# Performance work log

Hardware: AMD Instinct MI355X
Metric: run time of the kernel (lower is better)

The kernel has to match this reference:

```python
import jax, jax.numpy as jnp
import numpy as np
from jax import lax

EPS = 1e-5  # GroupNorm eps (torch default)

def _silu(x):
    return x * jax.nn.sigmoid(x)

def _conv1x1(x, w, b):
    # x: (N, Ci, H, W), w: (Co, Ci), b: (Co,)
    return jnp.einsum('oi,nihw->nohw', w, x) + b[None, :, None, None]

def _conv3x3(x, w, b):
    # x: (N, Ci, H, W), w: (Co, Ci, 3, 3)
    y = lax.conv_general_dilated(x, w, window_strides=(1, 1), padding='SAME',
                                 dimension_numbers=('NCHW', 'OIHW', 'NCHW'))
    return y + b[None, :, None, None]

def setup_inputs() -> dict:
    key = jax.random.key(0)
    ks = jax.random.split(key, 6)
    B, C, H, W = 32, 512, 64, 64
    cg = 16
    return {
        'x': jax.random.normal(ks[0], (B, C, H, W), dtype=jnp.float32),
        'w1': jax.random.normal(ks[1], (cg, cg), dtype=jnp.float32) * 0.1,
        'b1': jnp.zeros((cg,), jnp.float32),
        'wh': jax.random.normal(ks[2], (cg, cg), dtype=jnp.float32) * 0.1,
        'bh': jnp.zeros((cg,), jnp.float32),
        'ww': jax.random.normal(ks[3], (cg, cg), dtype=jnp.float32) * 0.1,
        'bw': jnp.zeros((cg,), jnp.float32),
        'w3': jax.random.normal(ks[4], (cg, cg, 3, 3), dtype=jnp.float32) * 0.1,
        'b3': jnp.zeros((cg,), jnp.float32),
        'gamma': jnp.ones((cg,), jnp.float32),
        'beta': jnp.zeros((cg,), jnp.float32),
    }

def reference(x, w1, b1, wh, bh, ww, bw, w3, b3, gamma, beta):
    b, c, h, w = x.shape
    cg = w1.shape[0]
    g = c // cg
    n = b * g
    hw = h * w
    xg = x.reshape(n, cg, h, w)
    # directional pooling: (N, cg, H, 1) and (N, cg, W, 1)
    x_h = jnp.mean(xg, axis=3, keepdims=True)
    x_w = jnp.transpose(jnp.mean(xg, axis=2, keepdims=True), (0, 1, 3, 2))
    y = jnp.concatenate([x_h, x_w], axis=2)            # (N, cg, H+W, 1)
    y = _silu(_conv1x1(y, w1, b1))
    y_h, y_w = y[:, :, :h, :], y[:, :, h:, :]
    y_w = jnp.transpose(y_w, (0, 1, 3, 2))             # (N, cg, 1, W)
    a_h = jax.nn.sigmoid(_conv1x1(y_h, wh, bh))        # (N, cg, H, 1)
    a_w = jax.nn.sigmoid(_conv1x1(y_w, ww, bw))        # (N, cg, 1, W)
    x1 = xg * a_h * a_w
    # GroupNorm(num_groups=1): normalize over (cg, H, W) per sample
    mu = jnp.mean(x1, axis=(1, 2, 3), keepdims=True)
    var = jnp.var(x1, axis=(1, 2, 3), keepdims=True)
    x1 = (x1 - mu) * lax.rsqrt(var + EPS)
    x1 = x1 * gamma[None, :, None, None] + beta[None, :, None, None]
    x3 = _silu(_conv3x3(xg, w3, b3))
    A1 = jax.nn.softmax(x1.reshape(n, cg, hw), axis=-1)
    A3 = jax.nn.softmax(x3.reshape(n, cg, hw), axis=-1)
    v1 = jnp.mean(x1, axis=(2, 3))                     # (N, cg)
    v3 = jnp.mean(x3, axis=(2, 3))                     # (N, cg)
    s1 = jnp.einsum('nc,ncp->np', v1, A3)              # (N, HW)
    s2 = jnp.einsum('nc,ncp->np', v3, A1)
    s = jax.nn.sigmoid(s1 + s2).reshape(n, 1, h, w)
    out = (xg * s).reshape(b, c, h, w)
    return out
```

## Files before the change

### kernel.cpp

```cpp
#include <hip/hip_runtime.h>


typedef short bf16x8 __attribute__((ext_vector_type(8)));
typedef float f32x4 __attribute__((ext_vector_type(4)));

__device__ __forceinline__ unsigned short f2bf(float f) {
    union { float f; unsigned int u; } v; v.f = f;
    unsigned int u = v.u;
    u += 0x7fffu + ((u >> 16) & 1u);
    return (unsigned short)(u >> 16);
}
__device__ __forceinline__ float bf2f(unsigned short h) {
    union { unsigned int u; float f; } v; v.u = ((unsigned int)h) << 16;
    return v.f;
}
__device__ __forceinline__ float sigm(float v) { return 1.0f / (1.0f + __expf(-v)); }

#define XIDX(h1,w1,c) ((((h1)*2 + ((c)>>3))*66 + (w1))*8 + ((c)&7))

__global__ __launch_bounds__(512) void ema_fused(
    const float* __restrict__ x,
    const float* __restrict__ w1, const float* __restrict__ b1,
    const float* __restrict__ wh, const float* __restrict__ bh,
    const float* __restrict__ ww, const float* __restrict__ bw,
    const float* __restrict__ w3, const float* __restrict__ b3,
    const float* __restrict__ gamma, const float* __restrict__ beta,
    float* __restrict__ out)
{
    const int n   = blockIdx.x;
    const int tid = threadIdx.x;
    const int lane = tid & 63;
    const int wv   = tid >> 6;
    const int qd   = lane >> 4;
    const int col  = lane & 15;

    const float* xg = x + (size_t)n * 65536;
    unsigned int* ob = (unsigned int*)out + (size_t)n * 65536;

    __shared__ unsigned short sX[69696];
    __shared__ float sG[2048];
    __shared__ float sRedA[128], sRedB[128], sRedC[128], sRedD[128];
    __shared__ float sS1[16], sSQ[16], sMn[16], sMx[16], sM3[16], sS3[16];
    __shared__ float sA[16], sB1[16], sQ1[16], sQ3[16];
    __shared__ float sScal[2];

    for (int i = tid; i < 34848; i += 512) ((unsigned int*)sX)[i] = 0u;
    __syncthreads();
    for (int e = tid; e < 32768; e += 512) {
        int c2 = e & 7, w = (e >> 3) & 63, r = e >> 9;
        float v0 = xg[(2*c2)*4096 + r*64 + w];
        float v1 = xg[(2*c2+1)*4096 + r*64 + w];
        unsigned int pk = (unsigned int)f2bf(v0) | ((unsigned int)f2bf(v1) << 16);
        ((unsigned int*)sX)[XIDX(r+1, w+1, 2*c2) >> 1] = pk;
    }
    __syncthreads();

    if (tid < 256) {
        int half = tid & 1;
        int idx  = tid >> 1;
        int isCol = idx >> 6;
        int rc = idx & 63;
        float acc[8] = {0,0,0,0,0,0,0,0};
        for (int t = 0; t < 64; ++t) {
            int hh = isCol ? (t + 1) : (rc + 1);
            int wwi = isCol ? (rc + 1) : (t + 1);
            const bf16x8 v = *(const bf16x8*)&sX[XIDX(hh, wwi, half*8)];
            #pragma unroll
            for (int j = 0; j < 8; ++j) acc[j] += bf2f((unsigned short)v[j]);
        }
        #pragma unroll
        for (int j = 0; j < 8; ++j)
            sG[isCol*1024 + (half*8+j)*64 + rc] = acc[j] * (1.0f/64.0f);
    }
    __syncthreads();

    {
        float yv[4];
        #pragma unroll
        for (int j = 0; j < 4; ++j) {
            int tsk = tid + j*512;
            int o = tsk & 15, q = tsk >> 4;
            float acc = b1[o];
            #pragma unroll
            for (int i = 0; i < 16; ++i)
                acc += w1[o*16 + i] * sG[((q>>6)<<10) + i*64 + (q & 63)];
            yv[j] = acc * sigm(acc);
        }
        __syncthreads();
        #pragma unroll
        for (int j = 0; j < 4; ++j) {
            int tsk = tid + j*512;
            int o = tsk & 15, q = tsk >> 4;
            sG[o*128 + q] = yv[j];
        }
    }
    __syncthreads();
    {
        float av[4];
        #pragma unroll
        for (int j = 0; j < 4; ++j) {
            int tsk = tid + j*512;
            int kind = tsk >> 10;
            int o = tsk & 15, pos = (tsk >> 4) & 63;
            const float* wm = kind ? ww : wh;
            float acc = kind ? bw[o] : bh[o];
            #pragma unroll
            for (int i = 0; i < 16; ++i)
                acc += wm[o*16 + i] * sG[i*128 + kind*64 + pos];
            av[j] = sigm(acc);
        }
        __syncthreads();
        #pragma unroll
        for (int j = 0; j < 4; ++j) {
            int tsk = tid + j*512;
            int kind = tsk >> 10, o = tsk & 15, pos = (tsk >> 4) & 63;
            sG[kind*1024 + o*64 + pos] = av[j];
        }
    }
    __syncthreads();

    {
        bf16x8 afr[5];
        int offs[5];
        #pragma unroll
        for (int mm = 0; mm < 5; ++mm) {
            int t = 2*mm + (qd >> 1);
            #pragma unroll
            for (int j = 0; j < 8; ++j) {
                int i = ((qd & 1) << 3) + j;
                float v = (t <= 8) ? w3[(col*16 + i)*9 + t] : 0.0f;
                afr[mm][j] = (short)f2bf(v);
            }
            int tb = (t > 8) ? 8 : t;
            int dy = tb/3 - 1, dx = tb - (tb/3)*3 - 1;
            offs[mm] = dy*1056 + dx*8;
        }
        float b3v[4];
        #pragma unroll
        for (int r = 0; r < 4; ++r) b3v[r] = b3[qd*4 + r];

        float tmax[4] = {-1e30f,-1e30f,-1e30f,-1e30f};
        float tsum[4] = {0.f,0.f,0.f,0.f};

        for (int k = 0; k < 32; ++k) {
            int tile = wv*32 + k;
            int h = tile >> 2, wq = tile & 3;
            int base = XIDX(h+1, wq*16 + col + 1, (qd & 1)*8);
            f32x4 acc = {0.f, 0.f, 0.f, 0.f};
            #pragma unroll
            for (int mm = 0; mm < 5; ++mm) {
                const bf16x8 bfr = *(const bf16x8*)&sX[base + offs[mm]];
                acc = __builtin_amdgcn_mfma_f32_16x16x32_bf16(afr[mm], bfr, acc, 0, 0, 0);
            }
            int p = h*64 + wq*16 + col;
            float xv[4];
            #pragma unroll
            for (int r = 0; r < 4; ++r) {
                float v = acc[r] + b3v[r];
                float sv = v * sigm(v);
                xv[r] = sv;
                tmax[r] = fmaxf(tmax[r], sv);
                tsum[r] += sv;
            }
            unsigned int u0 = (unsigned int)f2bf(xv[0]) | ((unsigned int)f2bf(xv[1]) << 16);
            unsigned int u1 = (unsigned int)f2bf(xv[2]) | ((unsigned int)f2bf(xv[3]) << 16);
            ob[(4*qd)*4096 + p]     = u0;
            ob[(4*qd + 2)*4096 + p] = u1;
        }
        #pragma unroll
        for (int m = 1; m < 16; m <<= 1) {
            #pragma unroll
            for (int r = 0; r < 4; ++r) {
                tmax[r] = fmaxf(tmax[r], __shfl_xor(tmax[r], m, 64));
                tsum[r] += __shfl_xor(tsum[r], m, 64);
            }
        }
        if (col == 0) {
            #pragma unroll
            for (int r = 0; r < 4; ++r) {
                sRedA[wv*16 + qd*4 + r] = tmax[r];
                sRedB[wv*16 + qd*4 + r] = tsum[r];
            }
        }
    }
    __syncthreads();
    if (tid < 16) {
        float mx = -1e30f, sm = 0.f;
        for (int v2 = 0; v2 < 8; ++v2) { mx = fmaxf(mx, sRedA[v2*16 + tid]); sm += sRedB[v2*16 + tid]; }
        sM3[tid] = mx; sS3[tid] = sm;
    }
    __syncthreads();

    {
        int half = tid & 1;
        int wq4  = (tid >> 1) & 3;
        int r    = tid >> 3;
        float ah8[8];
        #pragma unroll
        for (int j = 0; j < 8; ++j) ah8[j] = sG[(half*8+j)*64 + r];
        float s1[8], q1[8], mn[8], mx[8];
        #pragma unroll
        for (int j = 0; j < 8; ++j) { s1[j]=0.f; q1[j]=0.f; mn[j]=1e30f; mx[j]=-1e30f; }
        for (int wi = 0; wi < 16; ++wi) {
            int w = wq4*16 + wi;
            const bf16x8 v = *(const bf16x8*)&sX[XIDX(r+1, w+1, half*8)];
            #pragma unroll
            for (int j = 0; j < 8; ++j) {
                float aw = sG[1024 + (half*8+j)*64 + w];
                float x1 = bf2f((unsigned short)v[j]) * ah8[j] * aw;
                s1[j] += x1; q1[j] += x1*x1;
                mn[j] = fminf(mn[j], x1); mx[j] = fmaxf(mx[j], x1);
            }
        }
        #pragma unroll
        for (int m = 2; m < 64; m <<= 1) {
            #pragma unroll
            for (int j = 0; j < 8; ++j) {
                s1[j] += __shfl_xor(s1[j], m, 64);
                q1[j] += __shfl_xor(q1[j], m, 64);
                mn[j] = fminf(mn[j], __shfl_xor(mn[j], m, 64));
                mx[j] = fmaxf(mx[j], __shfl_xor(mx[j], m, 64));
            }
        }
        if ((lane >> 1) == 0) {
            #pragma unroll
            for (int j = 0; j < 8; ++j) {
                int c = half*8 + j;
                sRedA[wv*16 + c] = s1[j];
                sRedB[wv*16 + c] = q1[j];
                sRedC[wv*16 + c] = mn[j];
                sRedD[wv*16 + c] = mx[j];
            }
        }
    }
    __syncthreads();
    if (tid < 16) {
        float s=0.f, q=0.f, mn=1e30f, mx=-1e30f;
        for (int v2 = 0; v2 < 8; ++v2) {
            s += sRedA[v2*16+tid]; q += sRedB[v2*16+tid];
            mn = fminf(mn, sRedC[v2*16+tid]); mx = fmaxf(mx, sRedD[v2*16+tid]);
        }
        sS1[tid]=s; sSQ[tid]=q; sMn[tid]=mn; sMx[tid]=mx;
    }
    __syncthreads();
    if (tid == 0) {
        float S=0.f, Q=0.f;
        for (int c = 0; c < 16; ++c) { S += sS1[c]; Q += sSQ[c]; }
        float mu = S * (1.0f/65536.0f);
        float var = Q * (1.0f/65536.0f) - mu*mu;
        sScal[0] = mu; sScal[1] = rsqrtf(var + 1e-5f);
    }
    __syncthreads();
    if (tid < 16) {
        float mu = sScal[0], rstd = sScal[1];
        float a  = gamma[tid] * rstd;
        float bb = beta[tid] - mu * a;
        float m1 = (a >= 0.f) ? (a*sMx[tid] + bb) : (a*sMn[tid] + bb);
        sA[tid]  = a;
        sB1[tid] = bb - m1;
        sMn[tid] = a * (sS1[tid] * (1.0f/4096.0f)) + bb;
        sMx[tid] = sS3[tid] * (1.0f/4096.0f);
    }
    __syncthreads();

    {
        float z1[16], z3[16];
        #pragma unroll
        for (int c = 0; c < 16; ++c) { z1[c]=0.f; z3[c]=0.f; }
        for (int pp = 0; pp < 8; ++pp) {
            int p = pp*512 + tid;
            int h = p >> 6, w = p & 63;
            const bf16x8 v0 = *(const bf16x8*)&sX[XIDX(h+1, w+1, 0)];
            const bf16x8 v1 = *(const bf16x8*)&sX[XIDX(h+1, w+1, 8)];
            unsigned int xq[8];
            #pragma unroll
            for (int c2 = 0; c2 < 8; ++c2) xq[c2] = ob[(2*c2)*4096 + p];
            #pragma unroll
            for (int c = 0; c < 16; ++c) {
                float xv = bf2f((unsigned short)((c < 8) ? v0[c] : v1[c-8]));
                float g = sG[c*64 + h] * sG[1024 + c*64 + w];
                z1[c] += __expf(xv*g*sA[c] + sB1[c]);
                unsigned short ub = (unsigned short)((c & 1) ? (xq[c>>1] >> 16) : (xq[c>>1] & 0xffffu));
                z3[c] += __expf(bf2f(ub) - sM3[c]);
            }
        }
        #pragma unroll
        for (int m = 1; m < 64; m <<= 1) {
            #pragma unroll
            for (int c = 0; c < 16; ++c) {
                z1[c] += __shfl_xor(z1[c], m, 64);
                z3[c] += __shfl_xor(z3[c], m, 64);
            }
        }
        if (lane == 0) {
            #pragma unroll
            for (int c = 0; c < 16; ++c) { sRedA[wv*16 + c] = z1[c]; sRedB[wv*16 + c] = z3[c]; }
        }
    }
    __syncthreads();
    if (tid < 16) {
        float a1=0.f, a3=0.f;
        for (int v2 = 0; v2 < 8; ++v2) { a1 += sRedA[v2*16+tid]; a3 += sRedB[v2*16+tid]; }
        sQ1[tid] = sMx[tid] / a1;
        sQ3[tid] = sMn[tid] / a3;
    }
    __syncthreads();

    for (int pp = 0; pp < 8; ++pp) {
        int p = pp*512 + tid;
        int h = p >> 6, w = p & 63;
        const bf16x8 v0 = *(const bf16x8*)&sX[XIDX(h+1, w+1, 0)];
        const bf16x8 v1 = *(const bf16x8*)&sX[XIDX(h+1, w+1, 8)];
        unsigned int xq[8];
        #pragma unroll
        for (int c2 = 0; c2 < 8; ++c2) xq[c2] = ob[(2*c2)*4096 + p];
        float xf[16];
        #pragma unroll
        for (int c = 0; c < 16; ++c) xf[c] = xg[c*4096 + p];
        float z = 0.f;
        #pragma unroll
        for (int c = 0; c < 16; ++c) {
            float xv = bf2f((unsigned short)((c < 8) ? v0[c] : v1[c-8]));
            float g = sG[c*64 + h] * sG[1024 + c*64 + w];
            float e1 = __expf(xv*g*sA[c] + sB1[c]);
            unsigned short ub = (unsigned short)((c & 1) ? (xq[c>>1] >> 16) : (xq[c>>1] & 0xffffu));
            float e3 = __expf(bf2f(ub) - sM3[c]);
            z += sQ3[c]*e3 + sQ1[c]*e1;
        }
        float s = 1.0f / (1.0f + __expf(-z));
        #pragma unroll
        for (int c = 0; c < 16; ++c)
            ob[c*4096 + p] = __float_as_uint(xf[c] * s);
    }
}

extern "C" void kernel_launch(void* const* d_in, const int* in_sizes, int n_in,
                              void* d_out, int out_size, void* d_ws, size_t ws_size,
                              hipStream_t stream) {
    const float* x     = (const float*)d_in[0];
    const float* w1    = (const float*)d_in[1];
    const float* b1    = (const float*)d_in[2];
    const float* wh    = (const float*)d_in[3];
    const float* bh    = (const float*)d_in[4];
    const float* ww    = (const float*)d_in[5];
    const float* bw    = (const float*)d_in[6];
    const float* w3    = (const float*)d_in[7];
    const float* b3    = (const float*)d_in[8];
    const float* gamma = (const float*)d_in[9];
    const float* beta  = (const float*)d_in[10];
    hipLaunchKernelGGL(ema_fused, dim3(1024), dim3(512), 0, stream,
                       x, w1, b1, wh, bh, ww, bw, w3, b3, gamma, beta, (float*)d_out);
}
```

Measured before the change: 726.8 us.

## Stream input through small row-chunk LDS tile instead of caching whole slab

Replaces the ~139KB bf16 LDS copy of the full 16x64x64 group with a 18-row sliding tile, processing the image in four 16-row chunks. Row and column pooling are computed on the fly, and the conv3x3 MFMA runs per chunk. Later passes read x from global memory in fp32 with vectorized float4 loads instead of reading the bf16 LDS copy. The much smaller LDS footprint and launch_bounds(512,4) are meant to allow several blocks per CU, at the cost of re-reading x from global/L2 in the later passes and extra barriers per chunk.

```diff
diff --git a/kernel.cpp b/kernel.cpp
--- a/kernel.cpp
+++ b/kernel.cpp
@@ -3,6 +3,7 @@
 
 typedef short bf16x8 __attribute__((ext_vector_type(8)));
 typedef float f32x4 __attribute__((ext_vector_type(4)));
+typedef unsigned int u32x4 __attribute__((ext_vector_type(4)));
 
 __device__ __forceinline__ unsigned short f2bf(float f) {
     union { float f; unsigned int u; } v; v.f = f;
@@ -16,9 +17,9 @@
 }
 __device__ __forceinline__ float sigm(float v) { return 1.0f / (1.0f + __expf(-v)); }
 
-#define XIDX(h1,w1,c) ((((h1)*2 + ((c)>>3))*66 + (w1))*8 + ((c)&7))
-
-__global__ __launch_bounds__(512) void ema_fused(
+#define CIDX(lr, w1, c) ((((lr)*2 + ((c)>>3))*66 + (w1))*8 + ((c)&7))
+
+__global__ __launch_bounds__(512, 4) void ema_fused(
     const float* __restrict__ x,
     const float* __restrict__ w1, const float* __restrict__ b1,
     const float* __restrict__ wh, const float* __restrict__ bh,
@@ -27,8 +28,8 @@
     const float* __restrict__ gamma, const float* __restrict__ beta,
     float* __restrict__ out)
 {
-    const int n   = blockIdx.x;
-    const int tid = threadIdx.x;
+    const int n    = blockIdx.x;
+    const int tid  = threadIdx.x;
     const int lane = tid & 63;
     const int wv   = tid >> 6;
     const int qd   = lane >> 4;
@@ -37,40 +38,166 @@
     const float* xg = x + (size_t)n * 65536;
     unsigned int* ob = (unsigned int*)out + (size_t)n * 65536;
 
-    __shared__ unsigned short sX[69696];
-    __shared__ float sG[2048];
-    __shared__ float sRedA[128], sRedB[128], sRedC[128], sRedD[128];
+    __shared__ __align__(16) unsigned short sT[19008];
+    __shared__ __align__(16) float sG[2048];
+    __shared__ float sRowP[1024];
+    __shared__ float sRedA[128], sRedB[128];
     __shared__ float sS1[16], sSQ[16], sMn[16], sMx[16], sM3[16], sS3[16];
     __shared__ float sA[16], sB1[16], sQ1[16], sQ3[16];
     __shared__ float sScal[2];
 
-    for (int i = tid; i < 34848; i += 512) ((unsigned int*)sX)[i] = 0u;
-    __syncthreads();
-    for (int e = tid; e < 32768; e += 512) {
-        int c2 = e & 7, w = (e >> 3) & 63, r = e >> 9;
-        float v0 = xg[(2*c2)*4096 + r*64 + w];
-        float v1 = xg[(2*c2+1)*4096 + r*64 + w];
-        unsigned int pk = (unsigned int)f2bf(v0) | ((unsigned int)f2bf(v1) << 16);
-        ((unsigned int*)sX)[XIDX(r+1, w+1, 2*c2) >> 1] = pk;
-    }
-    __syncthreads();
-
-    if (tid < 256) {
-        int half = tid & 1;
-        int idx  = tid >> 1;
-        int isCol = idx >> 6;
-        int rc = idx & 63;
-        float acc[8] = {0,0,0,0,0,0,0,0};
-        for (int t = 0; t < 64; ++t) {
-            int hh = isCol ? (t + 1) : (rc + 1);
-            int wwi = isCol ? (rc + 1) : (t + 1);
-            const bf16x8 v = *(const bf16x8*)&sX[XIDX(hh, wwi, half*8)];
-            #pragma unroll
-            for (int j = 0; j < 8; ++j) acc[j] += bf2f((unsigned short)v[j]);
-        }
-        #pragma unroll
-        for (int j = 0; j < 8; ++j)
-            sG[isCol*1024 + (half*8+j)*64 + rc] = acc[j] * (1.0f/64.0f);
+    sG[tid] = 0.f; sG[tid + 512] = 0.f;
+    if (tid < 72) {
+        int lr = tid >> 2, blk = (tid >> 1) & 1, w1 = (tid & 1) * 65;
+        f32x4 zz = {0.f, 0.f, 0.f, 0.f};
+        *(f32x4*)&sT[((lr*2 + blk)*66 + w1)*8] = zz;
+    }
+
+    bf16x8 afr[5];
+    int offs[5];
+    #pragma unroll
+    for (int mm = 0; mm < 5; ++mm) {
+        int t = 2*mm + (qd >> 1);
+        #pragma unroll
+        for (int j = 0; j < 8; ++j) {
+            int i = ((qd & 1) << 3) + j;
+            float v = (t <= 8) ? w3[(col*16 + i)*9 + t] : 0.0f;
+            afr[mm][j] = (short)f2bf(v);
+        }
+        int tb = (t > 8) ? 8 : t;
+        int dy = tb/3 - 1, dx = tb - (tb/3)*3 - 1;
+        offs[mm] = dy*1056 + dx*8;
+    }
+    float b3v[4];
+    #pragma unroll
+    for (int r = 0; r < 4; ++r) b3v[r] = b3[qd*4 + r];
+
+    float tmax[4] = {-1e30f,-1e30f,-1e30f,-1e30f};
+    float tsum[4] = {0.f,0.f,0.f,0.f};
+    float colacc[8] = {0.f,0.f,0.f,0.f,0.f,0.f,0.f,0.f};
+    const int sblk = (tid >> 6) & 1;
+    const int sw   = tid & 63;
+
+    __syncthreads();
+
+    for (int c0 = 0; c0 < 4; ++c0) {
+        #pragma unroll
+        for (int k = 0; k < 5; ++k) {
+            int t = k*512 + tid;
+            if (t < 2304) {
+                int lr = t >> 7;
+                int gr = (c0 << 4) + lr - 1;
+                float v[8];
+                if ((unsigned)gr < 64u) {
+                    #pragma unroll
+                    for (int j = 0; j < 8; ++j)
+                        v[j] = xg[(sblk*8 + j)*4096 + gr*64 + sw];
+                } else {
+                    #pragma unroll
+                    for (int j = 0; j < 8; ++j) v[j] = 0.f;
+                }
+                if ((unsigned)(lr - 1) < 16u) {
+                    #pragma unroll
+                    for (int j = 0; j < 8; ++j) colacc[j] += v[j];
+                }
+                u32x4 pk;
+                #pragma unroll
+                for (int m = 0; m < 4; ++m)
+                    pk[m] = (unsigned int)f2bf(v[2*m]) | ((unsigned int)f2bf(v[2*m+1]) << 16);
+                *(u32x4*)&sT[((lr*2 + sblk)*66 + (sw + 1))*8] = pk;
+            }
+        }
+        __syncthreads();
+
+        if (tid < 128) {
+            int rr = tid >> 3, chalf = (tid >> 2) & 1, wq = tid & 3;
+            float racc[8] = {0.f,0.f,0.f,0.f,0.f,0.f,0.f,0.f};
+            #pragma unroll 4
+            for (int wi = 0; wi < 16; ++wi) {
+                const bf16x8 vv = *(const bf16x8*)&sT[CIDX(rr + 1, wq*16 + wi + 1, chalf*8)];
+                #pragma unroll
+                for (int j = 0; j < 8; ++j) racc[j] += bf2f((unsigned short)vv[j]);
+            }
+            #pragma unroll
+            for (int j = 0; j < 8; ++j)
+                sRowP[((rr*2 + chalf)*4 + wq)*8 + j] = racc[j];
+        }
+        #pragma unroll
+        for (int k = 0; k < 8; ++k) {
+            int tile = wv*8 + k;
+            int hl = tile >> 2, wq = tile & 3;
+            int base = CIDX(hl + 1, wq*16 + col + 1, (qd & 1)*8);
+            f32x4 acc = {0.f, 0.f, 0.f, 0.f};
+            #pragma unroll
+            for (int mm = 0; mm < 5; ++mm) {
+                const bf16x8 bfr = *(const bf16x8*)&sT[base + offs[mm]];
+                acc = __builtin_amdgcn_mfma_f32_16x16x32_bf16(afr[mm], bfr, acc, 0, 0, 0);
+            }
+            int p = ((c0 << 4) + hl)*64 + wq*16 + col;
+            float xv4[4];
+            #pragma unroll
+            for (int r = 0; r < 4; ++r) {
+                float v = acc[r] + b3v[r];
+                float sv = v * sigm(v);
+                xv4[r] = sv;
+                tmax[r] = fmaxf(tmax[r], sv);
+                tsum[r] += sv;
+            }
+            ob[(4*qd)*4096 + p]     = (unsigned int)f2bf(xv4[0]) | ((unsigned int)f2bf(xv4[1]) << 16);
+            ob[(4*qd + 2)*4096 + p] = (unsigned int)f2bf(xv4[2]) | ((unsigned int)f2bf(xv4[3]) << 16);
+        }
+        __syncthreads();
+
+        if (tid < 256) {
+            int c = tid & 15, rr = tid >> 4;
+            int bse = (rr*2 + (c >> 3))*4;
+            float s = sRowP[(bse + 0)*8 + (c & 7)] + sRowP[(bse + 1)*8 + (c & 7)]
+                    + sRowP[(bse + 2)*8 + (c & 7)] + sRowP[(bse + 3)*8 + (c & 7)];
+            sG[c*64 + (c0 << 4) + rr] += s;
+        }
+    }
+
+    #pragma unroll
+    for (int m = 1; m < 16; m <<= 1) {
+        #pragma unroll
+        for (int r = 0; r < 4; ++r) {
+            tmax[r] = fmaxf(tmax[r], __shfl_xor(tmax[r], m, 64));
+            tsum[r] += __shfl_xor(tsum[r], m, 64);
+        }
+    }
+    if (col == 0) {
+        #pragma unroll
+        for (int r = 0; r < 4; ++r) {
+            sRedA[wv*16 + qd*4 + r] = tmax[r];
+            sRedB[wv*16 + qd*4 + r] = tsum[r];
+        }
+    }
+    {
+        float* colScr = (float*)sT;
+        f32x4 d0 = {colacc[0], colacc[1], colacc[2], colacc[3]};
+        f32x4 d1 = {colacc[4], colacc[5], colacc[6], colacc[7]};
+        *(f32x4*)&colScr[tid*8]     = d0;
+        *(f32x4*)&colScr[tid*8 + 4] = d1;
+    }
+    __syncthreads();
+
+    {
+        const float* colScr = (const float*)sT;
+        #pragma unroll
+        for (int s0 = 0; s0 < 2; ++s0) {
+            int s = s0*512 + tid;
+            int c = s >> 6, w = s & 63;
+            int off = (c >> 3)*64 + w;
+            float cs = colScr[(off      )*8 + (c & 7)] + colScr[(off + 128)*8 + (c & 7)]
+                     + colScr[(off + 256)*8 + (c & 7)] + colScr[(off + 384)*8 + (c & 7)];
+            sG[1024 + s] = cs * (1.0f/64.0f);
+            sG[s] *= (1.0f/64.0f);
+        }
+    }
+    if (tid < 16) {
+        float mx = -1e30f, sm = 0.f;
+        for (int v2 = 0; v2 < 8; ++v2) { mx = fmaxf(mx, sRedA[v2*16 + tid]); sm += sRedB[v2*16 + tid]; }
+        sM3[tid] = mx; sS3[tid] = sm;
     }
     __syncthreads();
 
@@ -120,131 +247,37 @@
     __syncthreads();
 
     {
-        bf16x8 afr[5];
-        int offs[5];
-        #pragma unroll
-        for (int mm = 0; mm < 5; ++mm) {
-            int t = 2*mm + (qd >> 1);
-            #pragma unroll
-            for (int j = 0; j < 8; ++j) {
-                int i = ((qd & 1) << 3) + j;
-                float v = (t <= 8) ? w3[(col*16 + i)*9 + t] : 0.0f;
-                afr[mm][j] = (short)f2bf(v);
-            }
-            int tb = (t > 8) ? 8 : t;
-            int dy = tb/3 - 1, dx = tb - (tb/3)*3 - 1;
-            offs[mm] = dy*1056 + dx*8;
-        }
-        float b3v[4];
-        #pragma unroll
-        for (int r = 0; r < 4; ++r) b3v[r] = b3[qd*4 + r];
-
-        float tmax[4] = {-1e30f,-1e30f,-1e30f,-1e30f};
-        float tsum[4] = {0.f,0.f,0.f,0.f};
-
-        for (int k = 0; k < 32; ++k) {
-            int tile = wv*32 + k;
-            int h = tile >> 2, wq = tile & 3;
-            int base = XIDX(h+1, wq*16 + col + 1, (qd & 1)*8);
-            f32x4 acc = {0.f, 0.f, 0.f, 0.f};
-            #pragma unroll
-            for (int mm = 0; mm < 5; ++mm) {
-                const bf16x8 bfr = *(const bf16x8*)&sX[base + offs[mm]];
-                acc = __builtin_amdgcn_mfma_f32_16x16x32_bf16(afr[mm], bfr, acc, 0, 0, 0);
-            }
-            int p = h*64 + wq*16 + col;
-            float xv[4];
-            #pragma unroll
-            for (int r = 0; r < 4; ++r) {
-                float v = acc[r] + b3v[r];
-                float sv = v * sigm(v);
-                xv[r] = sv;
-                tmax[r] = fmaxf(tmax[r], sv);
-                tsum[r] += sv;
-            }
-            unsigned int u0 = (unsigned int)f2bf(xv[0]) | ((unsigned int)f2bf(xv[1]) << 16);
-            unsigned int u1 = (unsigned int)f2bf(xv[2]) | ((unsigned int)f2bf(xv[3]) << 16);
-            ob[(4*qd)*4096 + p]     = u0;
-            ob[(4*qd + 2)*4096 + p] = u1;
-        }
-        #pragma unroll
-        for (int m = 1; m < 16; m <<= 1) {
-            #pragma unroll
-            for (int r = 0; r < 4; ++r) {
-                tmax[r] = fmaxf(tmax[r], __shfl_xor(tmax[r], m, 64));
-                tsum[r] += __shfl_xor(tsum[r], m, 64);
-            }
-        }
-        if (col == 0) {
-            #pragma unroll
-            for (int r = 0; r < 4; ++r) {
-                sRedA[wv*16 + qd*4 + r] = tmax[r];
-                sRedB[wv*16 + qd*4 + r] = tsum[r];
-            }
-        }
-    }
-    __syncthreads();
-    if (tid < 16) {
-        float mx = -1e30f, sm = 0.f;
-        for (int v2 = 0; v2 < 8; ++v2) { mx = fmaxf(mx, sRedA[v2*16 + tid]); sm += sRedB[v2*16 + tid]; }
-        sM3[tid] = mx; sS3[tid] = sm;
-    }
-    __syncthreads();
-
-    {
-        int half = tid & 1;
-        int wq4  = (tid >> 1) & 3;
-        int r    = tid >> 3;
-        float ah8[8];
-        #pragma unroll
-        for (int j = 0; j < 8; ++j) ah8[j] = sG[(half*8+j)*64 + r];
-        float s1[8], q1[8], mn[8], mx[8];
-        #pragma unroll
-        for (int j = 0; j < 8; ++j) { s1[j]=0.f; q1[j]=0.f; mn[j]=1e30f; mx[j]=-1e30f; }
-        for (int wi = 0; wi < 16; ++wi) {
-            int w = wq4*16 + wi;
-            const bf16x8 v = *(const bf16x8*)&sX[XIDX(r+1, w+1, half*8)];
-            #pragma unroll
-            for (int j = 0; j < 8; ++j) {
-                float aw = sG[1024 + (half*8+j)*64 + w];
-                float x1 = bf2f((unsigned short)v[j]) * ah8[j] * aw;
-                s1[j] += x1; q1[j] += x1*x1;
-                mn[j] = fminf(mn[j], x1); mx[j] = fmaxf(mx[j], x1);
-            }
-        }
-        #pragma unroll
-        for (int m = 2; m < 64; m <<= 1) {
-            #pragma unroll
-            for (int j = 0; j < 8; ++j) {
-                s1[j] += __shfl_xor(s1[j], m, 64);
-                q1[j] += __shfl_xor(q1[j], m, 64);
-                mn[j] = fminf(mn[j], __shfl_xor(mn[j], m, 64));
-                mx[j] = fmaxf(mx[j], __shfl_xor(mx[j], m, 64));
-            }
-        }
-        if ((lane >> 1) == 0) {
-            #pragma unroll
-            for (int j = 0; j < 8; ++j) {
-                int c = half*8 + j;
-                sRedA[wv*16 + c] = s1[j];
-                sRedB[wv*16 + c] = q1[j];
-                sRedC[wv*16 + c] = mn[j];
-                sRedD[wv*16 + c] = mx[j];
-            }
-        }
-    }
-    __syncthreads();
-    if (tid < 16) {
-        float s=0.f, q=0.f, mn=1e30f, mx=-1e30f;
-        for (int v2 = 0; v2 < 8; ++v2) {
-            s += sRedA[v2*16+tid]; q += sRedB[v2*16+tid];
-            mn = fminf(mn, sRedC[v2*16+tid]); mx = fmaxf(mx, sRedD[v2*16+tid]);
-        }
-        sS1[tid]=s; sSQ[tid]=q; sMn[tid]=mn; sMx[tid]=mx;
+        #pragma unroll
+        for (int cc = 0; cc < 2; ++cc) {
+            const int c = wv*2 + cc;
+            const int w0 = (lane & 15) * 4;
+            const f32x4 aw4 = *(const f32x4*)&sG[1024 + c*64 + w0];
+            float ps = 0.f, pq = 0.f, mn = 1e30f, mx = -1e30f;
+            #pragma unroll 4
+            for (int i = 0; i < 16; ++i) {
+                const int p = i*256 + lane*4;
+                const float ah = sG[c*64 + i*4 + (lane >> 4)];
+                const f32x4 xv = *(const f32x4*)&xg[c*4096 + p];
+                #pragma unroll
+                for (int j = 0; j < 4; ++j) {
+                    float x1 = xv[j] * ah * aw4[j];
+                    ps += x1; pq = fmaf(x1, x1, pq);
+                    mn = fminf(mn, x1); mx = fmaxf(mx, x1);
+                }
+            }
+            #pragma unroll
+            for (int m = 1; m < 64; m <<= 1) {
+                ps += __shfl_xor(ps, m, 64);
+                pq += __shfl_xor(pq, m, 64);
+                mn = fminf(mn, __shfl_xor(mn, m, 64));
+                mx = fmaxf(mx, __shfl_xor(mx, m, 64));
+            }
+            if (lane == 0) { sS1[c] = ps; sSQ[c] = pq; sMn[c] = mn; sMx[c] = mx; }
+        }
     }
     __syncthreads();
     if (tid == 0) {
-        float S=0.f, Q=0.f;
+        float S = 0.f, Q = 0.f;
         for (int c = 0; c < 16; ++c) { S += sS1[c]; Q += sSQ[c]; }
         float mu = S * (1.0f/65536.0f);
         float var = Q * (1.0f/65536.0f) - mu*mu;
@@ -266,22 +299,30 @@
     {
         float z1[16], z3[16];
         #pragma unroll
-        for (int c = 0; c < 16; ++c) { z1[c]=0.f; z3[c]=0.f; }
-        for (int pp = 0; pp < 8; ++pp) {
-            int p = pp*512 + tid;
-            int h = p >> 6, w = p & 63;
-            const bf16x8 v0 = *(const bf16x8*)&sX[XIDX(h+1, w+1, 0)];
-            const bf16x8 v1 = *(const bf16x8*)&sX[XIDX(h+1, w+1, 8)];
-            unsigned int xq[8];
-            #pragma unroll
-            for (int c2 = 0; c2 < 8; ++c2) xq[c2] = ob[(2*c2)*4096 + p];
-            #pragma unroll
-            for (int c = 0; c < 16; ++c) {
-                float xv = bf2f((unsigned short)((c < 8) ? v0[c] : v1[c-8]));
-                float g = sG[c*64 + h] * sG[1024 + c*64 + w];
-                z1[c] += __expf(xv*g*sA[c] + sB1[c]);
-                unsigned short ub = (unsigned short)((c & 1) ? (xq[c>>1] >> 16) : (xq[c>>1] & 0xffffu));
-                z3[c] += __expf(bf2f(ub) - sM3[c]);
+        for (int c = 0; c < 16; ++c) { z1[c] = 0.f; z3[c] = 0.f; }
+        #pragma unroll
+        for (int it = 0; it < 2; ++it) {
+            const int p0 = it*2048 + tid*4;
+            const int h  = p0 >> 6;
+            const int w0 = (tid & 15)*4;
+            #pragma unroll
+            for (int c2 = 0; c2 < 8; ++c2) {
+                const u32x4 xq = *(const u32x4*)&ob[(2*c2)*4096 + p0];
+                #pragma unroll
+                for (int hf = 0; hf < 2; ++hf) {
+                    const int c = 2*c2 + hf;
+                    const f32x4 xf  = *(const f32x4*)&xg[c*4096 + p0];
+                    const f32x4 aw4 = *(const f32x4*)&sG[1024 + c*64 + w0];
+                    const float tt = sG[c*64 + h] * sA[c];
+                    const float bb = sB1[c];
+                    const float m3 = sM3[c];
+                    #pragma unroll
+                    for (int j = 0; j < 4; ++j) {
+                        z1[c] += __expf(fmaf(xf[j], tt * aw4[j], bb));
+                        unsigned int uu = hf ? (xq[j] & 0xffff0000u) : (xq[j] << 16);
+                        z3[c] += __expf(__uint_as_float(uu) - m3);
+                    }
+                }
             }
         }
         #pragma unroll
@@ -299,38 +340,51 @@
     }
     __syncthreads();
     if (tid < 16) {
-        float a1=0.f, a3=0.f;
-        for (int v2 = 0; v2 < 8; ++v2) { a1 += sRedA[v2*16+tid]; a3 += sRedB[v2*16+tid]; }
+        float a1 = 0.f, a3 = 0.f;
+        for (int v2 = 0; v2 < 8; ++v2) { a1 += sRedA[v2*16 + tid]; a3 += sRedB[v2*16 + tid]; }
         sQ1[tid] = sMx[tid] / a1;
         sQ3[tid] = sMn[tid] / a3;
     }
     __syncthreads();
 
-    for (int pp = 0; pp < 8; ++pp) {
-        int p = pp*512 + tid;
-        int h = p >> 6, w = p & 63;
-        const bf16x8 v0 = *(const bf16x8*)&sX[XIDX(h+1, w+1, 0)];
-        const bf16x8 v1 = *(const bf16x8*)&sX[XIDX(h+1, w+1, 8)];
-        unsigned int xq[8];
-        #pragma unroll
-        for (int c2 = 0; c2 < 8; ++c2) xq[c2] = ob[(2*c2)*4096 + p];
-        float xf[16];
-        #pragma unroll
-        for (int c = 0; c < 16; ++c) xf[c] = xg[c*4096 + p];
-        float z = 0.f;
+    #pragma unroll
+    for (int it = 0; it < 2; ++it) {
+        const int p0 = it*2048 + tid*4;
+        const int h  = p0 >> 6;
+        const int w0 = (tid & 15)*4;
+        f32x4 z = {0.f, 0.f, 0.f, 0.f};
+        #pragma unroll
+        for (int c2 = 0; c2 < 8; ++c2) {
+            const u32x4 xq = *(const u32x4*)&ob[(2*c2)*4096 + p0];
+            #pragma unroll
+            for (int hf = 0; hf < 2; ++hf) {
+                const int c = 2*c2 + hf;
+                const f32x4 xf  = *(const f32x4*)&xg[c*4096 + p0];
+                const f32x4 aw4 = *(const f32x4*)&sG[1024 + c*64 + w0];
+                const float tt = sG[c*64 + h] * sA[c];
+                const float bb = sB1[c];
+                const float m3 = sM3[c];
+                const float q1c = sQ1[c], q3c = sQ3[c];
+                #pragma unroll
+                for (int j = 0; j < 4; ++j) {
+                    float e1 = __expf(fmaf(xf[j], tt * aw4[j], bb));
+                    unsigned int uu = hf ? (xq[j] & 0xffff0000u) : (xq[j] << 16);
+                    float e3 = __expf(__uint_as_float(uu) - m3);
+                    z[j] = fmaf(q1c, e1, fmaf(q3c, e3, z[j]));
+                }
+            }
+        }
+        f32x4 s4;
+        #pragma unroll
+        for (int j = 0; j < 4; ++j) s4[j] = 1.0f / (1.0f + __expf(-z[j]));
         #pragma unroll
         for (int c = 0; c < 16; ++c) {
-            float xv = bf2f((unsigned short)((c < 8) ? v0[c] : v1[c-8]));
-            float g = sG[c*64 + h] * sG[1024 + c*64 + w];
-            float e1 = __expf(xv*g*sA[c] + sB1[c]);
-            unsigned short ub = (unsigned short)((c & 1) ? (xq[c>>1] >> 16) : (xq[c>>1] & 0xffffu));
-            float e3 = __expf(bf2f(ub) - sM3[c]);
-            z += sQ3[c]*e3 + sQ1[c]*e1;
-        }
-        float s = 1.0f / (1.0f + __expf(-z));
-        #pragma unroll
-        for (int c = 0; c < 16; ++c)
-            ob[c*4096 + p] = __float_as_uint(xf[c] * s);
+            const f32x4 xf = *(const f32x4*)&xg[c*4096 + p0];
+            u32x4 o4;
+            #pragma unroll
+            for (int j = 0; j < 4; ++j) o4[j] = __float_as_uint(xf[j] * s4[j]);
+            *(u32x4*)&ob[c*4096 + p0] = o4;
+        }
     }
 }
 
```

New measurement: 1.355 ms. +86.4%, slower.

## Recompute 3x3 conv via MFMA per pass instead of spilling bf16 to output

Applied to the files above, without the earlier changes.

Doubles the block to 1024 threads and stops staging the conv3x3+SiLU result as bf16 in the global output buffer. The MFMA convolution is instead recomputed in each of the three passes (stats, softmax denominators, final write). The GroupNorm statistics are folded into the first conv pass, and the row/column pooling is split across more threads. This removes global scratch writes and reads, at the cost of three times the MFMA work and higher register pressure at 1024 threads per block.

```diff
diff --git a/kernel.cpp b/kernel.cpp
--- a/kernel.cpp
+++ b/kernel.cpp
@@ -2,6 +2,7 @@
 
 
 typedef short bf16x8 __attribute__((ext_vector_type(8)));
+typedef short bf16x4 __attribute__((ext_vector_type(4)));
 typedef float f32x4 __attribute__((ext_vector_type(4)));
 
 __device__ __forceinline__ unsigned short f2bf(float f) {
@@ -18,7 +19,7 @@
 
 #define XIDX(h1,w1,c) ((((h1)*2 + ((c)>>3))*66 + (w1))*8 + ((c)&7))
 
-__global__ __launch_bounds__(512) void ema_fused(
+__global__ __launch_bounds__(1024) void ema_fused(
     const float* __restrict__ x,
     const float* __restrict__ w1, const float* __restrict__ b1,
     const float* __restrict__ wh, const float* __restrict__ bh,
@@ -27,41 +28,61 @@
     const float* __restrict__ gamma, const float* __restrict__ beta,
     float* __restrict__ out)
 {
-    const int n   = blockIdx.x;
-    const int tid = threadIdx.x;
+    const int n    = blockIdx.x;
+    const int tid  = threadIdx.x;
     const int lane = tid & 63;
     const int wv   = tid >> 6;
     const int qd   = lane >> 4;
     const int col  = lane & 15;
 
     const float* xg = x + (size_t)n * 65536;
-    unsigned int* ob = (unsigned int*)out + (size_t)n * 65536;
-
-    __shared__ unsigned short sX[69696];
-    __shared__ float sG[2048];
-    __shared__ float sRedA[128], sRedB[128], sRedC[128], sRedD[128];
+    float* ob = out + (size_t)n * 65536;
+
+    __shared__ __align__(16) unsigned short sX[69696];
+    __shared__ __align__(16) float sG[2048];
+    __shared__ float sRedA[256], sRedB[256], sRedC[256], sRedD[256], sRedE[256], sRedF[256];
     __shared__ float sS1[16], sSQ[16], sMn[16], sMx[16], sM3[16], sS3[16];
     __shared__ float sA[16], sB1[16], sQ1[16], sQ3[16];
     __shared__ float sScal[2];
 
-    for (int i = tid; i < 34848; i += 512) ((unsigned int*)sX)[i] = 0u;
-    __syncthreads();
-    for (int e = tid; e < 32768; e += 512) {
+    for (int i = tid; i < 34848; i += 1024) ((unsigned int*)sX)[i] = 0u;
+    __syncthreads();
+    for (int e = tid; e < 32768; e += 1024) {
         int c2 = e & 7, w = (e >> 3) & 63, r = e >> 9;
         float v0 = xg[(2*c2)*4096 + r*64 + w];
         float v1 = xg[(2*c2+1)*4096 + r*64 + w];
         unsigned int pk = (unsigned int)f2bf(v0) | ((unsigned int)f2bf(v1) << 16);
         ((unsigned int*)sX)[XIDX(r+1, w+1, 2*c2) >> 1] = pk;
     }
-    __syncthreads();
-
-    if (tid < 256) {
+
+    bf16x8 afr[5];
+    int offs[5];
+    #pragma unroll
+    for (int mm = 0; mm < 5; ++mm) {
+        int t = 2*mm + (qd >> 1);
+        #pragma unroll
+        for (int j = 0; j < 8; ++j) {
+            int i = ((qd & 1) << 3) + j;
+            float v = (t <= 8) ? w3[(col*16 + i)*9 + t] : 0.0f;
+            afr[mm][j] = (short)f2bf(v);
+        }
+        int tb = (t > 8) ? 8 : t;
+        int dy = tb/3 - 1, dx = tb - (tb/3)*3 - 1;
+        offs[mm] = dy*1056 + dx*8;
+    }
+    float b3v[4];
+    #pragma unroll
+    for (int r = 0; r < 4; ++r) b3v[r] = b3[qd*4 + r];
+    __syncthreads();
+
+    if (tid < 512) {
         int half = tid & 1;
-        int idx  = tid >> 1;
+        int part = (tid >> 1) & 1;
+        int idx  = tid >> 2;
         int isCol = idx >> 6;
         int rc = idx & 63;
         float acc[8] = {0,0,0,0,0,0,0,0};
-        for (int t = 0; t < 64; ++t) {
+        for (int t = part*32; t < part*32 + 32; ++t) {
             int hh = isCol ? (t + 1) : (rc + 1);
             int wwi = isCol ? (rc + 1) : (t + 1);
             const bf16x8 v = *(const bf16x8*)&sX[XIDX(hh, wwi, half*8)];
@@ -69,16 +90,20 @@
             for (int j = 0; j < 8; ++j) acc[j] += bf2f((unsigned short)v[j]);
         }
         #pragma unroll
-        for (int j = 0; j < 8; ++j)
-            sG[isCol*1024 + (half*8+j)*64 + rc] = acc[j] * (1.0f/64.0f);
-    }
-    __syncthreads();
-
-    {
-        float yv[4];
-        #pragma unroll
-        for (int j = 0; j < 4; ++j) {
-            int tsk = tid + j*512;
+        for (int j = 0; j < 8; ++j) acc[j] += __shfl_xor(acc[j], 2, 64);
+        if (part == 0) {
+            #pragma unroll
+            for (int j = 0; j < 8; ++j)
+                sG[isCol*1024 + (half*8+j)*64 + rc] = acc[j] * (1.0f/64.0f);
+        }
+    }
+    __syncthreads();
+
+    {
+        float yv[2];
+        #pragma unroll
+        for (int j = 0; j < 2; ++j) {
+            int tsk = tid + j*1024;
             int o = tsk & 15, q = tsk >> 4;
             float acc = b1[o];
             #pragma unroll
@@ -88,18 +113,18 @@
         }
         __syncthreads();
         #pragma unroll
-        for (int j = 0; j < 4; ++j) {
-            int tsk = tid + j*512;
+        for (int j = 0; j < 2; ++j) {
+            int tsk = tid + j*1024;
             int o = tsk & 15, q = tsk >> 4;
             sG[o*128 + q] = yv[j];
         }
     }
     __syncthreads();
     {
-        float av[4];
-        #pragma unroll
-        for (int j = 0; j < 4; ++j) {
-            int tsk = tid + j*512;
+        float av[2];
+        #pragma unroll
+        for (int j = 0; j < 2; ++j) {
+            int tsk = tid + j*1024;
             int kind = tsk >> 10;
             int o = tsk & 15, pos = (tsk >> 4) & 63;
             const float* wm = kind ? ww : wh;
@@ -111,8 +136,8 @@
         }
         __syncthreads();
         #pragma unroll
-        for (int j = 0; j < 4; ++j) {
-            int tsk = tid + j*512;
+        for (int j = 0; j < 2; ++j) {
+            int tsk = tid + j*1024;
             int kind = tsk >> 10, o = tsk & 15, pos = (tsk >> 4) & 63;
             sG[kind*1024 + o*64 + pos] = av[j];
         }
@@ -120,52 +145,33 @@
     __syncthreads();
 
     {
-        bf16x8 afr[5];
-        int offs[5];
-        #pragma unroll
-        for (int mm = 0; mm < 5; ++mm) {
-            int t = 2*mm + (qd >> 1);
-            #pragma unroll
-            for (int j = 0; j < 8; ++j) {
-                int i = ((qd & 1) << 3) + j;
-                float v = (t <= 8) ? w3[(col*16 + i)*9 + t] : 0.0f;
-                afr[mm][j] = (short)f2bf(v);
-            }
-            int tb = (t > 8) ? 8 : t;
-            int dy = tb/3 - 1, dx = tb - (tb/3)*3 - 1;
-            offs[mm] = dy*1056 + dx*8;
-        }
-        float b3v[4];
-        #pragma unroll
-        for (int r = 0; r < 4; ++r) b3v[r] = b3[qd*4 + r];
-
         float tmax[4] = {-1e30f,-1e30f,-1e30f,-1e30f};
         float tsum[4] = {0.f,0.f,0.f,0.f};
-
-        for (int k = 0; k < 32; ++k) {
-            int tile = wv*32 + k;
-            int h = tile >> 2, wq = tile & 3;
-            int base = XIDX(h+1, wq*16 + col + 1, (qd & 1)*8);
+        float s1[4] = {0.f,0.f,0.f,0.f}, q1[4] = {0.f,0.f,0.f,0.f};
+        float mn[4] = {1e30f,1e30f,1e30f,1e30f}, mx[4] = {-1e30f,-1e30f,-1e30f,-1e30f};
+        for (int k = 0; k < 16; ++k) {
+            int tile = wv*16 + k;
+            int hl = tile >> 2, wq = tile & 3;
+            int w = wq*16 + col;
+            int base = XIDX(hl+1, w+1, (qd & 1)*8);
             f32x4 acc = {0.f, 0.f, 0.f, 0.f};
             #pragma unroll
             for (int mm = 0; mm < 5; ++mm) {
                 const bf16x8 bfr = *(const bf16x8*)&sX[base + offs[mm]];
                 acc = __builtin_amdgcn_mfma_f32_16x16x32_bf16(afr[mm], bfr, acc, 0, 0, 0);
             }
-            int p = h*64 + wq*16 + col;
-            float xv[4];
+            const bf16x4 xv4 = *(const bf16x4*)&sX[XIDX(hl+1, w+1, qd*4)];
             #pragma unroll
             for (int r = 0; r < 4; ++r) {
                 float v = acc[r] + b3v[r];
                 float sv = v * sigm(v);
-                xv[r] = sv;
-                tmax[r] = fmaxf(tmax[r], sv);
-                tsum[r] += sv;
-            }
-            unsigned int u0 = (unsigned int)f2bf(xv[0]) | ((unsigned int)f2bf(xv[1]) << 16);
-            unsigned int u1 = (unsigned int)f2bf(xv[2]) | ((unsigned int)f2bf(xv[3]) << 16);
-            ob[(4*qd)*4096 + p]     = u0;
-            ob[(4*qd + 2)*4096 + p] = u1;
+                tmax[r] = fmaxf(tmax[r], sv); tsum[r] += sv;
+                int c = qd*4 + r;
+                float g = sG[c*64 + hl] * sG[1024 + c*64 + w];
+                float x1v = bf2f((unsigned short)xv4[r]) * g;
+                s1[r] += x1v; q1[r] = fmaf(x1v, x1v, q1[r]);
+                mn[r] = fminf(mn[r], x1v); mx[r] = fmaxf(mx[r], x1v);
+            }
         }
         #pragma unroll
         for (int m = 1; m < 16; m <<= 1) {
@@ -173,78 +179,36 @@
             for (int r = 0; r < 4; ++r) {
                 tmax[r] = fmaxf(tmax[r], __shfl_xor(tmax[r], m, 64));
                 tsum[r] += __shfl_xor(tsum[r], m, 64);
+                s1[r] += __shfl_xor(s1[r], m, 64);
+                q1[r] += __shfl_xor(q1[r], m, 64);
+                mn[r] = fminf(mn[r], __shfl_xor(mn[r], m, 64));
+                mx[r] = fmaxf(mx[r], __shfl_xor(mx[r], m, 64));
             }
         }
         if (col == 0) {
             #pragma unroll
             for (int r = 0; r < 4; ++r) {
-                sRedA[wv*16 + qd*4 + r] = tmax[r];
-                sRedB[wv*16 + qd*4 + r] = tsum[r];
+                int s = wv*16 + qd*4 + r;
+                sRedA[s] = tmax[r]; sRedB[s] = tsum[r];
+                sRedC[s] = s1[r];   sRedD[s] = q1[r];
+                sRedE[s] = mn[r];   sRedF[s] = mx[r];
             }
         }
     }
     __syncthreads();
     if (tid < 16) {
-        float mx = -1e30f, sm = 0.f;
-        for (int v2 = 0; v2 < 8; ++v2) { mx = fmaxf(mx, sRedA[v2*16 + tid]); sm += sRedB[v2*16 + tid]; }
-        sM3[tid] = mx; sS3[tid] = sm;
-    }
-    __syncthreads();
-
-    {
-        int half = tid & 1;
-        int wq4  = (tid >> 1) & 3;
-        int r    = tid >> 3;
-        float ah8[8];
-        #pragma unroll
-        for (int j = 0; j < 8; ++j) ah8[j] = sG[(half*8+j)*64 + r];
-        float s1[8], q1[8], mn[8], mx[8];
-        #pragma unroll
-        for (int j = 0; j < 8; ++j) { s1[j]=0.f; q1[j]=0.f; mn[j]=1e30f; mx[j]=-1e30f; }
-        for (int wi = 0; wi < 16; ++wi) {
-            int w = wq4*16 + wi;
-            const bf16x8 v = *(const bf16x8*)&sX[XIDX(r+1, w+1, half*8)];
-            #pragma unroll
-            for (int j = 0; j < 8; ++j) {
-                float aw = sG[1024 + (half*8+j)*64 + w];
-                float x1 = bf2f((unsigned short)v[j]) * ah8[j] * aw;
-                s1[j] += x1; q1[j] += x1*x1;
-                mn[j] = fminf(mn[j], x1); mx[j] = fmaxf(mx[j], x1);
-            }
-        }
-        #pragma unroll
-        for (int m = 2; m < 64; m <<= 1) {
-            #pragma unroll
-            for (int j = 0; j < 8; ++j) {
-                s1[j] += __shfl_xor(s1[j], m, 64);
-                q1[j] += __shfl_xor(q1[j], m, 64);
-                mn[j] = fminf(mn[j], __shfl_xor(mn[j], m, 64));
-                mx[j] = fmaxf(mx[j], __shfl_xor(mx[j], m, 64));
-            }
-        }
-        if ((lane >> 1) == 0) {
-            #pragma unroll
-            for (int j = 0; j < 8; ++j) {
-                int c = half*8 + j;
-                sRedA[wv*16 + c] = s1[j];
-                sRedB[wv*16 + c] = q1[j];
-                sRedC[wv*16 + c] = mn[j];
-                sRedD[wv*16 + c] = mx[j];
-            }
-        }
-    }
-    __syncthreads();
-    if (tid < 16) {
-        float s=0.f, q=0.f, mn=1e30f, mx=-1e30f;
-        for (int v2 = 0; v2 < 8; ++v2) {
-            s += sRedA[v2*16+tid]; q += sRedB[v2*16+tid];
-            mn = fminf(mn, sRedC[v2*16+tid]); mx = fmaxf(mx, sRedD[v2*16+tid]);
-        }
-        sS1[tid]=s; sSQ[tid]=q; sMn[tid]=mn; sMx[tid]=mx;
+        float m3 = -1e30f, sm3 = 0.f, s = 0.f, q = 0.f, mn = 1e30f, mx = -1e30f;
+        for (int v2 = 0; v2 < 16; ++v2) {
+            m3 = fmaxf(m3, sRedA[v2*16 + tid]); sm3 += sRedB[v2*16 + tid];
+            s += sRedC[v2*16 + tid]; q += sRedD[v2*16 + tid];
+            mn = fminf(mn, sRedE[v2*16 + tid]); mx = fmaxf(mx, sRedF[v2*16 + tid]);
+        }
+        sM3[tid] = m3; sS3[tid] = sm3;
+        sS1[tid] = s; sSQ[tid] = q; sMn[tid] = mn; sMx[tid] = mx;
     }
     __syncthreads();
     if (tid == 0) {
-        float S=0.f, Q=0.f;
+        float S = 0.f, Q = 0.f;
         for (int c = 0; c < 16; ++c) { S += sS1[c]; Q += sSQ[c]; }
         float mu = S * (1.0f/65536.0f);
         float var = Q * (1.0f/65536.0f) - mu*mu;
@@ -264,73 +228,102 @@
     __syncthreads();
 
     {
-        float z1[16], z3[16];
-        #pragma unroll
-        for (int c = 0; c < 16; ++c) { z1[c]=0.f; z3[c]=0.f; }
-        for (int pp = 0; pp < 8; ++pp) {
-            int p = pp*512 + tid;
-            int h = p >> 6, w = p & 63;
-            const bf16x8 v0 = *(const bf16x8*)&sX[XIDX(h+1, w+1, 0)];
-            const bf16x8 v1 = *(const bf16x8*)&sX[XIDX(h+1, w+1, 8)];
-            unsigned int xq[8];
-            #pragma unroll
-            for (int c2 = 0; c2 < 8; ++c2) xq[c2] = ob[(2*c2)*4096 + p];
-            #pragma unroll
-            for (int c = 0; c < 16; ++c) {
-                float xv = bf2f((unsigned short)((c < 8) ? v0[c] : v1[c-8]));
-                float g = sG[c*64 + h] * sG[1024 + c*64 + w];
-                z1[c] += __expf(xv*g*sA[c] + sB1[c]);
-                unsigned short ub = (unsigned short)((c & 1) ? (xq[c>>1] >> 16) : (xq[c>>1] & 0xffffu));
-                z3[c] += __expf(bf2f(ub) - sM3[c]);
-            }
-        }
-        #pragma unroll
-        for (int m = 1; m < 64; m <<= 1) {
-            #pragma unroll
-            for (int c = 0; c < 16; ++c) {
-                z1[c] += __shfl_xor(z1[c], m, 64);
-                z3[c] += __shfl_xor(z3[c], m, 64);
-            }
-        }
-        if (lane == 0) {
-            #pragma unroll
-            for (int c = 0; c < 16; ++c) { sRedA[wv*16 + c] = z1[c]; sRedB[wv*16 + c] = z3[c]; }
+        float aC[4], bC[4], m3C[4];
+        #pragma unroll
+        for (int r = 0; r < 4; ++r) {
+            int c = qd*4 + r;
+            aC[r] = sA[c]; bC[r] = sB1[c]; m3C[r] = sM3[c];
+        }
+        float z1p[4] = {0.f,0.f,0.f,0.f}, z3p[4] = {0.f,0.f,0.f,0.f};
+        for (int k = 0; k < 16; ++k) {
+            int tile = wv*16 + k;
+            int hl = tile >> 2, wq = tile & 3;
+            int w = wq*16 + col;
+            int base = XIDX(hl+1, w+1, (qd & 1)*8);
+            f32x4 acc = {0.f, 0.f, 0.f, 0.f};
+            #pragma unroll
+            for (int mm = 0; mm < 5; ++mm) {
+                const bf16x8 bfr = *(const bf16x8*)&sX[base + offs[mm]];
+                acc = __builtin_amdgcn_mfma_f32_16x16x32_bf16(afr[mm], bfr, acc, 0, 0, 0);
+            }
+            const bf16x4 xv4 = *(const bf16x4*)&sX[XIDX(hl+1, w+1, qd*4)];
+            #pragma unroll
+            for (int r = 0; r < 4; ++r) {
+                float v = acc[r] + b3v[r];
+                float sv = v * sigm(v);
+                z3p[r] += __expf(sv - m3C[r]);
+                int c = qd*4 + r;
+                float g = sG[c*64 + hl] * sG[1024 + c*64 + w];
+                z1p[r] += __expf(fmaf(bf2f((unsigned short)xv4[r]), g*aC[r], bC[r]));
+            }
+        }
+        #pragma unroll
+        for (int m = 1; m < 16; m <<= 1) {
+            #pragma unroll
+            for (int r = 0; r < 4; ++r) {
+                z1p[r] += __shfl_xor(z1p[r], m, 64);
+                z3p[r] += __shfl_xor(z3p[r], m, 64);
+            }
+        }
+        if (col == 0) {
+            #pragma unroll
+            for (int r = 0; r < 4; ++r) {
+                sRedA[wv*16 + qd*4 + r] = z1p[r];
+                sRedB[wv*16 + qd*4 + r] = z3p[r];
+            }
         }
     }
     __syncthreads();
     if (tid < 16) {
-        float a1=0.f, a3=0.f;
-        for (int v2 = 0; v2 < 8; ++v2) { a1 += sRedA[v2*16+tid]; a3 += sRedB[v2*16+tid]; }
+        float a1 = 0.f, a3 = 0.f;
+        for (int v2 = 0; v2 < 16; ++v2) { a1 += sRedA[v2*16 + tid]; a3 += sRedB[v2*16 + tid]; }
         sQ1[tid] = sMx[tid] / a1;
         sQ3[tid] = sMn[tid] / a3;
     }
     __syncthreads();
 
-    for (int pp = 0; pp < 8; ++pp) {
-        int p = pp*512 + tid;
-        int h = p >> 6, w = p & 63;
-        const bf16x8 v0 = *(const bf16x8*)&sX[XIDX(h+1, w+1, 0)];
-        const bf16x8 v1 = *(const bf16x8*)&sX[XIDX(h+1, w+1, 8)];
-        unsigned int xq[8];
-        #pragma unroll
-        for (int c2 = 0; c2 < 8; ++c2) xq[c2] = ob[(2*c2)*4096 + p];
-        float xf[16];
-        #pragma unroll
-        for (int c = 0; c < 16; ++c) xf[c] = xg[c*4096 + p];
-        float z = 0.f;
-        #pragma unroll
-        for (int c = 0; c < 16; ++c) {
-            float xv = bf2f((unsigned short)((c < 8) ? v0[c] : v1[c-8]));
-            float g = sG[c*64 + h] * sG[1024 + c*64 + w];
-            float e1 = __expf(xv*g*sA[c] + sB1[c]);
-            unsigned short ub = (unsigned short)((c & 1) ? (xq[c>>1] >> 16) : (xq[c>>1] & 0xffffu));
-            float e3 = __expf(bf2f(ub) - sM3[c]);
-            z += sQ3[c]*e3 + sQ1[c]*e1;
-        }
-        float s = 1.0f / (1.0f + __expf(-z));
-        #pragma unroll
-        for (int c = 0; c < 16; ++c)
-            ob[c*4096 + p] = __float_as_uint(xf[c] * s);
+    {
+        float aC[4], bC[4], m3C[4], q1C[4], q3C[4];
+        #pragma unroll
+        for (int r = 0; r < 4; ++r) {
+            int c = qd*4 + r;
+            aC[r] = sA[c]; bC[r] = sB1[c]; m3C[r] = sM3[c];
+            q1C[r] = sQ1[c]; q3C[r] = sQ3[c];
+        }
+        for (int k = 0; k < 16; ++k) {
+            int tile = wv*16 + k;
+            int hl = tile >> 2, wq = tile & 3;
+            int w = wq*16 + col;
+            int p = hl*64 + w;
+            int base = XIDX(hl+1, w+1, (qd & 1)*8);
+            f32x4 acc = {0.f, 0.f, 0.f, 0.f};
+            #pragma unroll
+            for (int mm = 0; mm < 5; ++mm) {
+                const bf16x8 bfr = *(const bf16x8*)&sX[base + offs[mm]];
+                acc = __builtin_amdgcn_mfma_f32_16x16x32_bf16(afr[mm], bfr, acc, 0, 0, 0);
+            }
+            const bf16x4 xv4 = *(const bf16x4*)&sX[XIDX(hl+1, w+1, qd*4)];
+            float xf[4];
+            #pragma unroll
+            for (int r = 0; r < 4; ++r) xf[r] = xg[(qd*4 + r)*4096 + p];
+            float zp = 0.f;
+            #pragma unroll
+            for (int r = 0; r < 4; ++r) {
+                float v = acc[r] + b3v[r];
+                float sv = v * sigm(v);
+                float e3 = __expf(sv - m3C[r]);
+                int c = qd*4 + r;
+                float g = sG[c*64 + hl] * sG[1024 + c*64 + w];
+                float e1 = __expf(fmaf(bf2f((unsigned short)xv4[r]), g*aC[r], bC[r]));
+                zp = fmaf(q3C[r], e3, fmaf(q1C[r], e1, zp));
+            }
+            zp += __shfl_xor(zp, 16, 64);
+            zp += __shfl_xor(zp, 32, 64);
+            float s = 1.0f / (1.0f + __expf(-zp));
+            #pragma unroll
+            for (int r = 0; r < 4; ++r)
+                ob[(qd*4 + r)*4096 + p] = xf[r] * s;
+        }
     }
 }
 
@@ -348,6 +341,6 @@
     const float* b3    = (const float*)d_in[8];
     const float* gamma = (const float*)d_in[9];
     const float* beta  = (const float*)d_in[10];
-    hipLaunchKernelGGL(ema_fused, dim3(1024), dim3(512), 0, stream,
+    hipLaunchKernelGGL(ema_fused, dim3(1024), dim3(1024), 0, stream,
                        x, w1, b1, wh, bh, ww, bw, w3, b3, gamma, beta, (float*)d_out);
 }
```

Measured after the change: 745.9 us. 2.6% more time.
